# Performance work log

Hardware: AMD Instinct MI355X
Metric: run time of the kernel (lower is better)

## Reference

```python
import jax, jax.numpy as jnp
import numpy as np

N, E, F_IN = 12288, 196608, 1433


def setup_inputs() -> dict:
    key = jax.random.key(0)
    ks = jax.random.split(key, 11)
    inp = {
        "x": jax.random.normal(ks[0], (N, F_IN), dtype=jnp.float32),
        "edge_index": jax.random.randint(ks[1], (2, E), 0, N, dtype=jnp.int64),
        "W1": jax.random.normal(ks[2], (F_IN, 32), dtype=jnp.float32) * 0.02,
        "b1": jnp.zeros((32,), dtype=jnp.float32),
        "Wl": jax.random.normal(ks[3], (32, 16), dtype=jnp.float32) * 0.1,
        "bl": jnp.zeros((16,), dtype=jnp.float32),
        "Wr": jax.random.normal(ks[4], (32, 16), dtype=jnp.float32) * 0.1,
        "br": jnp.zeros((16,), dtype=jnp.float32),
        "W3": jax.random.normal(ks[5], (16, 7), dtype=jnp.float32) * 0.1,
        "b3": jnp.zeros((7,), dtype=jnp.float32),
    }
    return inp


def reference(x, edge_index, W1, b1, Wl, bl, Wr, br, W3, b3):
    n = x.shape[0]
    loops = jnp.arange(n, dtype=edge_index.dtype)
    row = jnp.concatenate([edge_index[0], loops])  # [E+N]
    col = jnp.concatenate([edge_index[1], loops])

    # ---- GCN layer: dense symmetric-normalized adjacency (faithful to original) ----
    # degree computed over the col index of self-looped edges
    deg = jnp.zeros((n,), dtype=x.dtype).at[col].add(1.0)
    dis = jnp.where(deg > 0, deg ** -0.5, 0.0)  # inf -> 0 guard
    A = jnp.zeros((n, n), dtype=x.dtype).at[row, col].add(1.0)  # dense A-hat
    A_norm = dis[:, None] * A * dis[None, :]  # D^-1/2 A D^-1/2
    h = (A_norm @ x) @ W1 + b1
    h = jax.nn.relu(h)  # [N, 32]

    # ---- GraphSAGE layer: mean over neighbors j with edge (i -> j) ----
    src, dst = edge_index[0], edge_index[1]
    agg_sum = jax.ops.segment_sum(h[dst], src, num_segments=n)  # [N, 32]
    cnt = jax.ops.segment_sum(jnp.ones((src.shape[0],), dtype=h.dtype), src, num_segments=n)
    agg = jnp.where(cnt[:, None] > 0, agg_sum / jnp.maximum(cnt, 1.0)[:, None], 0.0)
    out = jax.nn.relu(h @ Wl + bl + agg @ Wr + br)  # [N, 16]
    out = out / (jnp.linalg.norm(out, axis=1, keepdims=True) + 1e-6)

    # ---- head: linear + dropout(eval: identity) + softmax ----
    logits = out @ W3 + b3  # [N, 7]
    return jax.nn.softmax(logits, axis=1)
```

## Files before the change

kernel.cpp:

```cpp
#include <hip/hip_runtime.h>
#include <hip/hip_bf16.h>
#include <math.h>

#define GN 12288
#define GE 196608
#define GK 1433
#define GC 32
#define CAP 64
#define BSTR 136
#define NSPLIT 12
#define KCHUNK 128
#define GEMMB (96 * NSPLIT)
#define EDGEB 768

typedef __attribute__((ext_vector_type(8))) short bf16x8;
typedef __attribute__((ext_vector_type(4))) float f32x4;

static __device__ inline unsigned short f2bf(float f) {
    unsigned u = __float_as_uint(f);
    unsigned r = (u + 0x7fffu + ((u >> 16) & 1u)) >> 16;
    return (unsigned short)r;
}
static __device__ inline float bf2f(unsigned short h) {
    return __uint_as_float(((unsigned)h) << 16);
}

__global__ __launch_bounds__(256) void fused_kernel(const float* __restrict__ x,
                                                    const float* __restrict__ W1,
                                                    const int* __restrict__ ei,
                                                    float* __restrict__ xw,
                                                    unsigned* __restrict__ cnt,
                                                    unsigned* __restrict__ deg,
                                                    unsigned* __restrict__ adjF) {
    int t = threadIdx.x, bid = blockIdx.x;

    if (bid >= GEMMB) {
        int e = (bid - GEMMB) * 256 + t;
        int src = ei[e];
        int dst = ei[GE + e];
        unsigned pos = atomicAdd(&cnt[src], 1u);
        if (pos < CAP) adjF[(unsigned)src * CAP + pos] = (unsigned)dst;
        atomicAdd(&deg[dst], 1u);
        return;
    }

    __shared__ unsigned short Bh[32 * BSTR], Bl[32 * BSTR];
    int lane = t & 63, w = t >> 6;
    int quad = lane >> 4, l15 = lane & 15;
    int row0 = (bid % 96) * 128;
    int ks = bid / 96;
    int k0 = ks * KCHUNK;
    int kend = min(GK, k0 + KCHUNK);
    f32x4 acc[2][2] = {};
    const float* xr0 = x + (size_t)(row0 + w * 32 + l15) * GK;
    const float* xr1 = xr0 + 16 * GK;

    for (int ksb = k0; ksb < kend; ksb += 128) {
        __syncthreads();
        #pragma unroll
        for (int e = 0; e < 16; ++e) {
            int idx = e * 256 + t;
            int kk = idx >> 5, c = idx & 31;
            int kg = ksb + kk;
            float f = (kg < kend) ? W1[(size_t)kg * GC + c] : 0.f;
            unsigned short hh = f2bf(f);
            unsigned short ll = f2bf(f - bf2f(hh));
            Bh[c * BSTR + kk] = hh;
            Bl[c * BSTR + kk] = ll;
        }
        __syncthreads();
        int kbe = min(128, kend - ksb);
        #pragma unroll 2
        for (int kb2 = 0; kb2 < kbe; kb2 += 32) {
            int kq = ksb + kb2 + quad * 8;
            float af0[8], af1[8];
            if (kq + 8 <= GK) {
                #pragma unroll
                for (int j = 0; j < 8; ++j) { af0[j] = xr0[kq + j]; af1[j] = xr1[kq + j]; }
            } else {
                #pragma unroll
                for (int j = 0; j < 8; ++j) {
                    bool v = (kq + j) < GK;
                    af0[j] = v ? xr0[kq + j] : 0.f;
                    af1[j] = v ? xr1[kq + j] : 0.f;
                }
            }
            bf16x8 ah[2], al[2];
            #pragma unroll
            for (int j = 0; j < 8; ++j) {
                unsigned short h0 = f2bf(af0[j]);
                ah[0][j] = (short)h0; al[0][j] = (short)f2bf(af0[j] - bf2f(h0));
                unsigned short h1 = f2bf(af1[j]);
                ah[1][j] = (short)h1; al[1][j] = (short)f2bf(af1[j] - bf2f(h1));
            }
            bf16x8 bh[2], bl_[2];
            #pragma unroll
            for (int nt = 0; nt < 2; ++nt) {
                int c = nt * 16 + l15;
                bh[nt]  = *(bf16x8*)&Bh[c * BSTR + kb2 + quad * 8];
                bl_[nt] = *(bf16x8*)&Bl[c * BSTR + kb2 + quad * 8];
            }
            #pragma unroll
            for (int mt = 0; mt < 2; ++mt)
                #pragma unroll
                for (int nt = 0; nt < 2; ++nt) {
                    acc[mt][nt] = __builtin_amdgcn_mfma_f32_16x16x32_bf16(ah[mt], bh[nt],  acc[mt][nt], 0, 0, 0);
                    acc[mt][nt] = __builtin_amdgcn_mfma_f32_16x16x32_bf16(ah[mt], bl_[nt], acc[mt][nt], 0, 0, 0);
                    acc[mt][nt] = __builtin_amdgcn_mfma_f32_16x16x32_bf16(al[mt], bh[nt],  acc[mt][nt], 0, 0, 0);
                }
        }
    }
    #pragma unroll
    for (int mt = 0; mt < 2; ++mt)
        #pragma unroll
        for (int i = 0; i < 4; ++i) {
            int row = row0 + w * 32 + mt * 16 + quad * 4 + i;
            float* po = xw + (size_t)row * GC;
            atomicAdd(&po[l15], acc[mt][0][i]);
            atomicAdd(&po[16 + l15], acc[mt][1][i]);
        }
}

__global__ __launch_bounds__(256) void gcn_kernel(const float* __restrict__ xw,
                                                  const unsigned* __restrict__ deg,
                                                  const unsigned* __restrict__ cnt,
                                                  const unsigned* __restrict__ adjF,
                                                  const float* __restrict__ b1,
                                                  float* __restrict__ h) {
    int w = threadIdx.x >> 6;
    int lane = threadIdx.x & 63;
    int i = blockIdx.x * 4 + w;
    int f = lane & 31, half = lane >> 5;
    unsigned cl = min(cnt[i], (unsigned)CAP);
    const unsigned* ai = adjF + (unsigned)i * CAP;
    float acc = 0.f;
    for (unsigned j = half; j < cl; j += 8) {
        unsigned lim = cl - 1;
        unsigned j1 = j + 2, j2 = j + 4, j3 = j + 6;
        unsigned d0 = ai[j];
        unsigned d1 = ai[min(j1, lim)];
        unsigned d2 = ai[min(j2, lim)];
        unsigned d3 = ai[min(j3, lim)];
        float m1 = j1 < cl ? 1.f : 0.f;
        float m2 = j2 < cl ? 1.f : 0.f;
        float m3 = j3 < cl ? 1.f : 0.f;
        acc += xw[(size_t)d0 * GC + f] * rsqrtf((float)(deg[d0] + 1u));
        acc += m1 * xw[(size_t)d1 * GC + f] * rsqrtf((float)(deg[d1] + 1u));
        acc += m2 * xw[(size_t)d2 * GC + f] * rsqrtf((float)(deg[d2] + 1u));
        acc += m3 * xw[(size_t)d3 * GC + f] * rsqrtf((float)(deg[d3] + 1u));
    }
    acc += __shfl_xor(acc, 32, 64);
    float disi = rsqrtf((float)(deg[i] + 1u));
    float v = b1[f] + disi * (disi * xw[(size_t)i * GC + f] + acc);
    if (half == 0) h[(size_t)i * GC + f] = fmaxf(v, 0.f);
}

__global__ __launch_bounds__(256) void sage_kernel(const float* __restrict__ h,
                                                   const unsigned* __restrict__ cnt,
                                                   const unsigned* __restrict__ adjF,
                                                   const float* __restrict__ Wl,
                                                   const float* __restrict__ bl,
                                                   const float* __restrict__ Wr,
                                                   const float* __restrict__ br,
                                                   const float* __restrict__ W3,
                                                   const float* __restrict__ b3,
                                                   float* __restrict__ out) {
    __shared__ float sh[4][64];
    __shared__ float so[4][16];
    int w = threadIdx.x >> 6, lane = threadIdx.x & 63;
    int i = blockIdx.x * 4 + w;
    int f = lane & 31, half = lane >> 5;
    unsigned ci = cnt[i];
    unsigned cl = min(ci, (unsigned)CAP);
    const unsigned* ai = adjF + (unsigned)i * CAP;
    float acc = 0.f;
    for (unsigned j = half; j < cl; j += 8) {
        unsigned lim = cl - 1;
        unsigned j1 = j + 2, j2 = j + 4, j3 = j + 6;
        unsigned d0 = ai[j];
        unsigned d1 = ai[min(j1, lim)];
        unsigned d2 = ai[min(j2, lim)];
        unsigned d3 = ai[min(j3, lim)];
        float m1 = j1 < cl ? 1.f : 0.f;
        float m2 = j2 < cl ? 1.f : 0.f;
        float m3 = j3 < cl ? 1.f : 0.f;
        acc += h[(size_t)d0 * GC + f];
        acc += m1 * h[(size_t)d1 * GC + f];
        acc += m2 * h[(size_t)d2 * GC + f];
        acc += m3 * h[(size_t)d3 * GC + f];
    }
    acc += __shfl_xor(acc, 32, 64);
    float agg = ci ? acc / (float)ci : 0.f;
    float hv = h[(size_t)i * GC + f];
    if (half == 0) { sh[w][f] = hv; sh[w][32 + f] = agg; }
    __syncthreads();
    int c = lane;
    float hid = 0.f;
    if (c < 16) {
        hid = bl[c] + br[c];
        #pragma unroll
        for (int ff = 0; ff < 32; ++ff)
            hid += sh[w][ff] * Wl[ff * 16 + c] + sh[w][32 + ff] * Wr[ff * 16 + c];
        hid = fmaxf(hid, 0.f);
    }
    float n2 = hid * hid;
    n2 += __shfl_xor(n2, 1, 64);
    n2 += __shfl_xor(n2, 2, 64);
    n2 += __shfl_xor(n2, 4, 64);
    n2 += __shfl_xor(n2, 8, 64);
    float o = hid / (sqrtf(n2) + 1e-6f);
    if (c < 16) so[w][c] = o;
    __syncthreads();
    float logit = -INFINITY;
    if (lane < 7) {
        logit = b3[lane];
        #pragma unroll
        for (int cc = 0; cc < 16; ++cc) logit += so[w][cc] * W3[cc * 7 + lane];
    }
    float m = logit;
    m = fmaxf(m, __shfl_xor(m, 1, 64));
    m = fmaxf(m, __shfl_xor(m, 2, 64));
    m = fmaxf(m, __shfl_xor(m, 4, 64));
    float e = expf(logit - m);
    float s = e;
    s += __shfl_xor(s, 1, 64);
    s += __shfl_xor(s, 2, 64);
    s += __shfl_xor(s, 4, 64);
    if (lane < 7) out[(size_t)i * 7 + lane] = e / s;
}

extern "C" void kernel_launch(void* const* d_in, const int* in_sizes, int n_in,
                              void* d_out, int out_size, void* d_ws, size_t ws_size,
                              hipStream_t stream) {
    const float* x  = (const float*)d_in[0];
    const int*   ei = (const int*)d_in[1];
    const float* W1 = (const float*)d_in[2];
    const float* b1 = (const float*)d_in[3];
    const float* Wl = (const float*)d_in[4];
    const float* bl = (const float*)d_in[5];
    const float* Wr = (const float*)d_in[6];
    const float* br = (const float*)d_in[7];
    const float* W3 = (const float*)d_in[8];
    const float* b3 = (const float*)d_in[9];
    float* out = (float*)d_out;

    char* ws = (char*)d_ws;
    const size_t S = (size_t)GN * GC * 4;
    float*    xw   = (float*)(ws);
    unsigned* cnt  = (unsigned*)(ws + S);
    unsigned* deg  = cnt + GN;
    float*    h    = (float*)((char*)(deg + GN));
    unsigned* adjF = (unsigned*)((char*)h + S);

    hipMemsetAsync(ws, 0, S + 2 * (size_t)GN * 4, stream);
    fused_kernel<<<GEMMB + EDGEB, 256, 0, stream>>>(x, W1, ei, xw, cnt, deg, adjF);
    gcn_kernel<<<GN / 4, 256, 0, stream>>>(xw, deg, cnt, adjF, b1, h);
    sage_kernel<<<GN / 4, 256, 0, stream>>>(h, cnt, adjF, Wl, bl, Wr, br, W3, b3, out);
}
```

Baseline: 167.1 us.

## Prepack W1 into bf16 hi/lo once and split K within block instead of atomics

```diff
diff --git a/kernel.cpp b/kernel.cpp
--- a/kernel.cpp
+++ b/kernel.cpp
@@ -1,5 +1,4 @@
 #include <hip/hip_runtime.h>
-#include <hip/hip_bf16.h>
 #include <math.h>
 
 #define GN 12288
@@ -7,27 +6,55 @@
 #define GK 1433
 #define GC 32
 #define CAP 64
-#define BSTR 136
-#define NSPLIT 12
-#define KCHUNK 128
-#define GEMMB (96 * NSPLIT)
+#define NCHUNK 45
+#define NGRP 180
+#define GEMMB 768
 #define EDGEB 768
+#define PACKB 23
+#define ZEROB 96
 
 typedef __attribute__((ext_vector_type(8))) short bf16x8;
 typedef __attribute__((ext_vector_type(4))) float f32x4;
 
 static __device__ inline unsigned short f2bf(float f) {
     unsigned u = __float_as_uint(f);
-    unsigned r = (u + 0x7fffu + ((u >> 16) & 1u)) >> 16;
-    return (unsigned short)r;
+    return (unsigned short)((u + 0x7fffu + ((u >> 16) & 1u)) >> 16);
 }
 static __device__ inline float bf2f(unsigned short h) {
     return __uint_as_float(((unsigned)h) << 16);
 }
 
+__global__ __launch_bounds__(256) void prep_kernel(const float* __restrict__ W1,
+                                                   unsigned* __restrict__ zbuf,
+                                                   unsigned short* __restrict__ Whb,
+                                                   unsigned short* __restrict__ Wlb) {
+    int t = threadIdx.x, b = blockIdx.x;
+    if (b < PACKB) {
+        int idx = b * 256 + t;
+        if (idx < NGRP * GC) {
+            int g = idx >> 5, c = idx & 31;
+            bf16x8 vh, vl;
+            #pragma unroll
+            for (int j = 0; j < 8; ++j) {
+                int k = g * 8 + j;
+                float f = (k < GK) ? W1[(size_t)k * GC + c] : 0.f;
+                unsigned short hh = f2bf(f);
+                vh[j] = (short)hh;
+                vl[j] = (short)f2bf(f - bf2f(hh));
+            }
+            *(bf16x8*)(Whb + (size_t)idx * 8) = vh;
+            *(bf16x8*)(Wlb + (size_t)idx * 8) = vl;
+        }
+    } else {
+        int idx = (b - PACKB) * 256 + t;
+        zbuf[idx] = 0u;
+    }
+}
+
 __global__ __launch_bounds__(256) void fused_kernel(const float* __restrict__ x,
-                                                    const float* __restrict__ W1,
                                                     const int* __restrict__ ei,
+                                                    const unsigned short* __restrict__ Whb,
+                                                    const unsigned short* __restrict__ Wlb,
                                                     float* __restrict__ xw,
                                                     unsigned* __restrict__ cnt,
                                                     unsigned* __restrict__ deg,
@@ -44,81 +71,73 @@
         return;
     }
 
-    __shared__ unsigned short Bh[32 * BSTR], Bl[32 * BSTR];
+    __shared__ float red[4][16][32];
     int lane = t & 63, w = t >> 6;
     int quad = lane >> 4, l15 = lane & 15;
-    int row0 = (bid % 96) * 128;
-    int ks = bid / 96;
-    int k0 = ks * KCHUNK;
-    int kend = min(GK, k0 + KCHUNK);
-    f32x4 acc[2][2] = {};
-    const float* xr0 = x + (size_t)(row0 + w * 32 + l15) * GK;
-    const float* xr1 = xr0 + 16 * GK;
-
-    for (int ksb = k0; ksb < kend; ksb += 128) {
-        __syncthreads();
-        #pragma unroll
-        for (int e = 0; e < 16; ++e) {
-            int idx = e * 256 + t;
-            int kk = idx >> 5, c = idx & 31;
-            int kg = ksb + kk;
-            float f = (kg < kend) ? W1[(size_t)kg * GC + c] : 0.f;
-            unsigned short hh = f2bf(f);
-            unsigned short ll = f2bf(f - bf2f(hh));
-            Bh[c * BSTR + kk] = hh;
-            Bl[c * BSTR + kk] = ll;
-        }
-        __syncthreads();
-        int kbe = min(128, kend - ksb);
-        #pragma unroll 2
-        for (int kb2 = 0; kb2 < kbe; kb2 += 32) {
-            int kq = ksb + kb2 + quad * 8;
-            float af0[8], af1[8];
-            if (kq + 8 <= GK) {
-                #pragma unroll
-                for (int j = 0; j < 8; ++j) { af0[j] = xr0[kq + j]; af1[j] = xr1[kq + j]; }
-            } else {
-                #pragma unroll
-                for (int j = 0; j < 8; ++j) {
-                    bool v = (kq + j) < GK;
-                    af0[j] = v ? xr0[kq + j] : 0.f;
-                    af1[j] = v ? xr1[kq + j] : 0.f;
-                }
-            }
-            bf16x8 ah[2], al[2];
-            #pragma unroll
-            for (int j = 0; j < 8; ++j) {
-                unsigned short h0 = f2bf(af0[j]);
-                ah[0][j] = (short)h0; al[0][j] = (short)f2bf(af0[j] - bf2f(h0));
-                unsigned short h1 = f2bf(af1[j]);
-                ah[1][j] = (short)h1; al[1][j] = (short)f2bf(af1[j] - bf2f(h1));
-            }
-            bf16x8 bh[2], bl_[2];
-            #pragma unroll
-            for (int nt = 0; nt < 2; ++nt) {
-                int c = nt * 16 + l15;
-                bh[nt]  = *(bf16x8*)&Bh[c * BSTR + kb2 + quad * 8];
-                bl_[nt] = *(bf16x8*)&Bl[c * BSTR + kb2 + quad * 8];
-            }
-            #pragma unroll
-            for (int mt = 0; mt < 2; ++mt)
-                #pragma unroll
-                for (int nt = 0; nt < 2; ++nt) {
-                    acc[mt][nt] = __builtin_amdgcn_mfma_f32_16x16x32_bf16(ah[mt], bh[nt],  acc[mt][nt], 0, 0, 0);
-                    acc[mt][nt] = __builtin_amdgcn_mfma_f32_16x16x32_bf16(ah[mt], bl_[nt], acc[mt][nt], 0, 0, 0);
-                    acc[mt][nt] = __builtin_amdgcn_mfma_f32_16x16x32_bf16(al[mt], bh[nt],  acc[mt][nt], 0, 0, 0);
-                }
-        }
-    }
+    int row = bid * 16 + l15;
+    const float* xr = x + (size_t)row * GK;
+    f32x4 acc0 = {}, acc1 = {};
+    int qs = w * 12;
+    int qe = min(NCHUNK, qs + 12);
+
+    float aA[8], aB[8];
+    bf16x8 hA0, hA1, lA0, lA1, hB0, hB1, lB0, lB1;
+
+#define LOADX(A8, q) { \
+    int kq = (q) * 32 + quad * 8; \
+    const float* p = xr + kq; \
+    if (kq + 8 <= GK) { \
+        _Pragma("unroll") for (int j = 0; j < 8; ++j) A8[j] = p[j]; \
+    } else { \
+        _Pragma("unroll") for (int j = 0; j < 8; ++j) A8[j] = (kq + j < GK) ? p[j] : 0.f; \
+    } }
+
+#define LOADW(H0, H1, L0, L1, q) { \
+    int g = (q) * 4 + quad; \
+    H0 = *(const bf16x8*)(Whb + (size_t)g * 256 + l15 * 8); \
+    H1 = *(const bf16x8*)(Whb + (size_t)g * 256 + 128 + l15 * 8); \
+    L0 = *(const bf16x8*)(Wlb + (size_t)g * 256 + l15 * 8); \
+    L1 = *(const bf16x8*)(Wlb + (size_t)g * 256 + 128 + l15 * 8); \
+    }
+
+#define COMP(A8, H0, H1, L0, L1) { \
+    bf16x8 ah, al; \
+    _Pragma("unroll") for (int j = 0; j < 8; ++j) { \
+        unsigned short hh = f2bf(A8[j]); \
+        ah[j] = (short)hh; \
+        al[j] = (short)f2bf(A8[j] - bf2f(hh)); \
+    } \
+    acc0 = __builtin_amdgcn_mfma_f32_16x16x32_bf16(ah, H0, acc0, 0, 0, 0); \
+    acc1 = __builtin_amdgcn_mfma_f32_16x16x32_bf16(ah, H1, acc1, 0, 0, 0); \
+    acc0 = __builtin_amdgcn_mfma_f32_16x16x32_bf16(ah, L0, acc0, 0, 0, 0); \
+    acc1 = __builtin_amdgcn_mfma_f32_16x16x32_bf16(ah, L1, acc1, 0, 0, 0); \
+    acc0 = __builtin_amdgcn_mfma_f32_16x16x32_bf16(al, H0, acc0, 0, 0, 0); \
+    acc1 = __builtin_amdgcn_mfma_f32_16x16x32_bf16(al, H1, acc1, 0, 0, 0); \
+    }
+
+    int q = qs;
+    LOADX(aA, q); LOADW(hA0, hA1, lA0, lA1, q);
+    while (true) {
+        if (q + 1 < qe) { LOADX(aB, q + 1); LOADW(hB0, hB1, lB0, lB1, q + 1); }
+        COMP(aA, hA0, hA1, lA0, lA1);
+        ++q; if (q >= qe) break;
+        if (q + 1 < qe) { LOADX(aA, q + 1); LOADW(hA0, hA1, lA0, lA1, q + 1); }
+        COMP(aB, hB0, hB1, lB0, lB1);
+        ++q; if (q >= qe) break;
+    }
+
     #pragma unroll
-    for (int mt = 0; mt < 2; ++mt)
-        #pragma unroll
-        for (int i = 0; i < 4; ++i) {
-            int row = row0 + w * 32 + mt * 16 + quad * 4 + i;
-            float* po = xw + (size_t)row * GC;
-            atomicAdd(&po[l15], acc[mt][0][i]);
-            atomicAdd(&po[16 + l15], acc[mt][1][i]);
-        }
+    for (int i = 0; i < 4; ++i) {
+        red[w][quad * 4 + i][l15] = acc0[i];
+        red[w][quad * 4 + i][16 + l15] = acc1[i];
+    }
+    __syncthreads();
+    int r0 = t >> 5, c0 = t & 31;
+    float s0 = red[0][r0][c0] + red[1][r0][c0] + red[2][r0][c0] + red[3][r0][c0];
+    int r1 = r0 + 8;
+    float s1 = red[0][r1][c0] + red[1][r1][c0] + red[2][r1][c0] + red[3][r1][c0];
+    xw[(size_t)bid * 512 + t] = s0;
+    xw[(size_t)bid * 512 + 256 + t] = s1;
 }
 
 __global__ __launch_bounds__(256) void gcn_kernel(const float* __restrict__ xw,
@@ -249,11 +268,13 @@
     float*    xw   = (float*)(ws);
     unsigned* cnt  = (unsigned*)(ws + S);
     unsigned* deg  = cnt + GN;
-    float*    h    = (float*)((char*)(deg + GN));
+    float*    h    = (float*)(deg + GN);
     unsigned* adjF = (unsigned*)((char*)h + S);
-
-    hipMemsetAsync(ws, 0, S + 2 * (size_t)GN * 4, stream);
-    fused_kernel<<<GEMMB + EDGEB, 256, 0, stream>>>(x, W1, ei, xw, cnt, deg, adjF);
+    unsigned short* Whb = (unsigned short*)((char*)adjF + (size_t)GN * CAP * 4);
+    unsigned short* Wlb = Whb + (size_t)NGRP * GC * 8;
+
+    prep_kernel<<<PACKB + ZEROB, 256, 0, stream>>>(W1, cnt, Whb, Wlb);
+    fused_kernel<<<GEMMB + EDGEB, 256, 0, stream>>>(x, ei, Whb, Wlb, xw, cnt, deg, adjF);
     gcn_kernel<<<GN / 4, 256, 0, stream>>>(xw, deg, cnt, adjF, b1, h);
     sage_kernel<<<GN / 4, 256, 0, stream>>>(h, cnt, adjF, Wl, bl, Wr, br, W3, b3, out);
 }
```

Result: no change. 164.7 us (-1.4%).
